# Kernel tuning notes

Hardware: AMD Instinct MI355X
Metric: run time of the kernel (lower is better)

## Reference

```python
import jax, jax.numpy as jnp
import numpy as np

# module hyperparameters (from init_kwargs)
STRIDE, PAD, DIL = 1, 1, 1
GROUPS, DG = 1, 1
KH, KW = 3, 3
CIN, COUT = 256, 256


def _mdcn_forward(x, offset, mask, weight, bias):
    B, C, H, W = x.shape
    Cout = weight.shape[0]
    K = KH * KW
    Ho = (H + 2 * PAD - (DIL * (KH - 1) + 1)) // STRIDE + 1
    Wo = (W + 2 * PAD - (DIL * (KW - 1) + 1)) // STRIDE + 1
    Cg = C // DG

    # offset channel layout: ((g*K + k)*2 + {0: dy, 1: dx})
    off = offset.reshape(B, DG, KH, KW, 2, Ho, Wo)
    base_y = (jnp.arange(Ho) * STRIDE - PAD)[None, :] + DIL * jnp.arange(KH)[:, None]  # [KH,Ho]
    base_x = (jnp.arange(Wo) * STRIDE - PAD)[None, :] + DIL * jnp.arange(KW)[:, None]  # [KW,Wo]
    sy = base_y[None, None, :, None, :, None].astype(x.dtype) + off[:, :, :, :, 0]  # [B,DG,KH,KW,Ho,Wo]
    sx = base_x[None, None, None, :, None, :].astype(x.dtype) + off[:, :, :, :, 1]

    y0f = jnp.floor(sy); x0f = jnp.floor(sx)
    wy = sy - y0f; wx = sx - x0f
    y0 = y0f.astype(jnp.int32); x0 = x0f.astype(jnp.int32)

    xg = x.reshape(B, DG, Cg, H * W)

    def corner(yc, xc, w):
        valid = (yc >= 0) & (yc < H) & (xc >= 0) & (xc < W)
        idx = jnp.clip(yc, 0, H - 1) * W + jnp.clip(xc, 0, W - 1)  # [B,DG,KH,KW,Ho,Wo]
        v = jnp.take_along_axis(xg, idx.reshape(B, DG, 1, -1), axis=3)  # [B,DG,Cg,K*Ho*Wo]
        v = v.reshape(B, DG, Cg, KH, KW, Ho, Wo)
        return v * (w * valid.astype(x.dtype))[:, :, None]

    val = (corner(y0, x0, (1 - wy) * (1 - wx))
           + corner(y0, x0 + 1, (1 - wy) * wx)
           + corner(y0 + 1, x0, wy * (1 - wx))
           + corner(y0 + 1, x0 + 1, wy * wx))  # [B,DG,Cg,KH,KW,Ho,Wo]

    cols = val * mask.reshape(B, DG, 1, KH, KW, Ho, Wo)
    cols = cols.reshape(B, GROUPS, (C // GROUPS) * K, Ho * Wo)
    wg = weight.reshape(GROUPS, Cout // GROUPS, (C // GROUPS) * K)
    out = jnp.einsum('gok,bgkp->bgop', wg, cols).reshape(B, Cout, Ho, Wo)
    return out + bias[None, :, None, None]


def setup_inputs() -> dict:
    key = jax.random.key(0)
    k1, k2, k3, k4 = jax.random.split(key, 4)
    B, H, W = 4, 64, 64
    x = jax.random.normal(k1, (B, CIN, H, W), dtype=jnp.float32)
    offset = jax.random.normal(k2, (B, 2 * DG * KH * KW, H, W), dtype=jnp.float32)
    mask = jax.random.uniform(k3, (B, DG * KH * KW, H, W), dtype=jnp.float32)
    stdv = 1.0 / np.sqrt(CIN * KH * KW)
    weight = jax.random.uniform(k4, (COUT, CIN // GROUPS, KH, KW), dtype=jnp.float32,
                                minval=-stdv, maxval=stdv)
    bias = jnp.zeros((COUT,), dtype=jnp.float32)
    return {"x": x, "offset": offset, "mask": mask, "weight": weight, "bias": bias}


def reference(x, offset, mask, weight, bias):
    return _mdcn_forward(x, offset, mask, weight, bias)
```

## Files before the change

kernel.cpp:

```cpp
#include <hip/hip_runtime.h>
#include <hip/hip_bf16.h>
#include <stdint.h>

#define KDIM 2304

typedef __bf16 bf16_t;
typedef bf16_t bf16x8 __attribute__((ext_vector_type(8)));
typedef float f32x4 __attribute__((ext_vector_type(4)));
typedef float f32x2 __attribute__((ext_vector_type(2)));

__device__ __forceinline__ float b2f_lo(uint32_t u) {
  union { uint32_t i; float f; } c; c.i = u << 16; return c.f;
}
__device__ __forceinline__ float b2f_hi(uint32_t u) {
  union { uint32_t i; float f; } c; c.i = u & 0xffff0000u; return c.f;
}
__device__ __forceinline__ uint32_t pk_bf16(float a, float b) {
  __hip_bfloat162 h = __float22bfloat162_rn(make_float2(a, b));
  union { __hip_bfloat162 h; uint32_t u; } c; c.h = h; return c.u;
}

__global__ __launch_bounds__(256) void k_prep(const float* __restrict__ x,
                                              uint16_t* __restrict__ xt,
                                              const float* __restrict__ w,
                                              uint16_t* __restrict__ wt2) {
  int tid = threadIdx.x;
  if (blockIdx.x < 2048) {
    __shared__ float tile[32][65];
    int b = blockIdx.x >> 9;
    int cgrp = (blockIdx.x >> 6) & 7;
    int sgrp = blockIdx.x & 63;
    int c0 = cgrp << 5, s0 = sgrp << 6;
#pragma unroll
    for (int it = 0; it < 2; ++it) {
      int f = tid + it * 256;
      int rr = f >> 4, col = (f & 15) << 2;
      float4 v = *(const float4*)&x[((size_t)(b * 256 + c0 + rr)) * 4096 + s0 + col];
      tile[rr][col + 0] = v.x;
      tile[rr][col + 1] = v.y;
      tile[rr][col + 2] = v.z;
      tile[rr][col + 3] = v.w;
    }
    __syncthreads();
    int sp = tid >> 2, cg = tid & 3;
    uint4 o;
    o.x = pk_bf16(tile[cg * 8 + 0][sp], tile[cg * 8 + 1][sp]);
    o.y = pk_bf16(tile[cg * 8 + 2][sp], tile[cg * 8 + 3][sp]);
    o.z = pk_bf16(tile[cg * 8 + 4][sp], tile[cg * 8 + 5][sp]);
    o.w = pk_bf16(tile[cg * 8 + 6][sp], tile[cg * 8 + 7][sp]);
    *(uint4*)&xt[((size_t)b * 4096 + s0 + sp) * 256 + c0 + cg * 8] = o;
  } else {
    __shared__ float wl[2304];
    int row = blockIdx.x - 2048;
    const float* wrow = w + (size_t)row * KDIM;
    for (int i2 = tid; i2 < 2304; i2 += 256) wl[i2] = wrow[i2];
    __syncthreads();
    int strip = row >> 4, r16 = row & 15;
    for (int c = tid; c < 288; c += 256) {
      int tap = c >> 5, rem = c & 31;
      int w64 = rem >> 3, kh = (rem >> 2) & 1, seg = rem & 3;
      int i = tap * 4 + w64;
      int cin0 = w64 * 64 + kh * 32 + seg * 8;
      int lanex = seg * 16 + r16;
      uint16_t* dst = wt2 + (size_t)i * 16384 + (size_t)(strip * 128 + kh * 64 + lanex) * 8;
      uint4 o;
      o.x = pk_bf16(wl[(cin0 + 0) * 9 + tap], wl[(cin0 + 1) * 9 + tap]);
      o.y = pk_bf16(wl[(cin0 + 2) * 9 + tap], wl[(cin0 + 3) * 9 + tap]);
      o.z = pk_bf16(wl[(cin0 + 4) * 9 + tap], wl[(cin0 + 5) * 9 + tap]);
      o.w = pk_bf16(wl[(cin0 + 6) * 9 + tap], wl[(cin0 + 7) * 9 + tap]);
      *(uint4*)dst = o;
    }
  }
}

__device__ __forceinline__ void mk_corners(int tap, int p, int ho,
                                           const float* s_off, const float* s_msk,
                                           float cw[4], int cpo[4]) {
  int kh = tap / 3, kw = tap - kh * 3;
  float dy = s_off[(2 * tap) * 64 + p];
  float dx = s_off[(2 * tap + 1) * 64 + p];
  float mm = s_msk[tap * 64 + p];
  float sy = (float)(ho - 1 + kh) + dy;
  float sx = (float)(p - 1 + kw) + dx;
  float fy = floorf(sy), fx = floorf(sx);
  int y0 = (int)fy, x0 = (int)fx;
  float wy = sy - fy, wx = sx - fx;
#pragma unroll
  for (int cy = 0; cy < 2; ++cy) {
#pragma unroll
    for (int cx = 0; cx < 2; ++cx) {
      int y = y0 + cy, xx = x0 + cx;
      float wgt = (cy ? wy : 1.f - wy) * (cx ? wx : 1.f - wx) * mm;
      bool v = ((unsigned)y < 64u) && ((unsigned)xx < 64u);
      wgt = v ? wgt : 0.f;
      int yc = min(max(y, 0), 63), xc = min(max(xx, 0), 63);
      cw[cy * 2 + cx] = wgt;
      cpo[cy * 2 + cx] = ((yc << 6) + xc) * 256;
    }
  }
}

__global__ __launch_bounds__(1024, 4) void k_fused(const uint16_t* __restrict__ xt,
                                                   const uint16_t* __restrict__ wt2,
                                                   const float* __restrict__ off,
                                                   const float* __restrict__ msk,
                                                   const float* __restrict__ bias,
                                                   float* __restrict__ out) {
  __shared__ __align__(16) uint16_t Bs[2][64][64];
  __shared__ float s_off[18 * 64];
  __shared__ float s_msk[9 * 64];

  int tid = threadIdx.x;
  int swz = ((int)blockIdx.x & 7) * 32 + ((int)blockIdx.x >> 3);
  int b = swz >> 6, ho = swz & 63;

  const float* offb = off + (size_t)b * 18 * 4096 + ho * 64;
  for (int i = tid; i < 18 * 64; i += 1024)
    s_off[i] = offb[(size_t)(i >> 6) * 4096 + (i & 63)];
  const float* mskb = msk + (size_t)b * 9 * 4096 + ho * 64;
  for (int i = tid; i < 9 * 64; i += 1024)
    s_msk[i] = mskb[(size_t)(i >> 6) * 4096 + (i & 63)];

  int lane = tid & 63, wv = tid >> 6;
  int wm = wv >> 1, wn = wv & 1;
  int q = lane >> 4, r = lane & 15;
  int p = tid >> 4, cg = tid & 15;
  const uint16_t* xtb = xt + (size_t)b * 4096 * 256 + cg * 4;
  int bcol = (((cg >> 1) ^ (p & 7)) << 3) + ((cg & 1) << 2);

  f32x4 acc[2][2];
#pragma unroll
  for (int mi = 0; mi < 2; ++mi)
#pragma unroll
    for (int ni = 0; ni < 2; ++ni) acc[mi][ni] = f32x4{0.f, 0.f, 0.f, 0.f};

  __syncthreads();

  float cw[4];
  int cpo[4];
  uint2 dnv[4];
  bf16x8 AFA[2][2], AFB[2][2];

  int c0 = (q ^ (r & 7)) << 3;
  int c1 = c0 ^ 32;
  int rb0 = (wn * 32 + r) * 64;

  mk_corners(0, p, ho, s_off, s_msk, cw, cpo);
#pragma unroll
  for (int c = 0; c < 4; ++c) dnv[c] = *(const uint2*)(xtb + cpo[c]);
  {
    const uint16_t* wp = wt2 + wm * 2048 + lane * 8;
    AFA[0][0] = *(const bf16x8*)(wp);
    AFA[0][1] = *(const bf16x8*)(wp + 512);
    AFA[1][0] = *(const bf16x8*)(wp + 1024);
    AFA[1][1] = *(const bf16x8*)(wp + 1536);
  }
  {
    f32x2 a0 = {0.f, 0.f}, a1 = {0.f, 0.f};
#pragma unroll
    for (int c = 0; c < 4; ++c) {
      f32x2 wc = {cw[c], cw[c]};
      a0 += wc * f32x2{b2f_lo(dnv[c].x), b2f_hi(dnv[c].x)};
      a1 += wc * f32x2{b2f_lo(dnv[c].y), b2f_hi(dnv[c].y)};
    }
    uint2 o;
    o.x = pk_bf16(a0.x, a0.y);
    o.y = pk_bf16(a1.x, a1.y);
    *(uint2*)&Bs[0][p][bcol] = o;
  }
  __syncthreads();

#define BODY(I, AFC, AFN, DOMK, DODNV, DOAF, DOBL)                              \
  {                                                                             \
    if (DOMK) mk_corners(((I) + 1) >> 2, p, ho, s_off, s_msk, cw, cpo);         \
    if (DODNV) {                                                                \
      const int chw = (((I) + 1) & 3) << 6;                                     \
      dnv[0] = *(const uint2*)(xtb + cpo[0] + chw);                             \
      dnv[1] = *(const uint2*)(xtb + cpo[1] + chw);                             \
      dnv[2] = *(const uint2*)(xtb + cpo[2] + chw);                             \
      dnv[3] = *(const uint2*)(xtb + cpo[3] + chw);                             \
    }                                                                           \
    if (DOAF) {                                                                 \
      const uint16_t* wp = wt2 + (size_t)((I) + 1) * 16384 + wm * 2048 + lane * 8; \
      AFN[0][0] = *(const bf16x8*)(wp);                                         \
      AFN[0][1] = *(const bf16x8*)(wp + 512);                                   \
      AFN[1][0] = *(const bf16x8*)(wp + 1024);                                  \
      AFN[1][1] = *(const bf16x8*)(wp + 1536);                                  \
    }                                                                           \
    {                                                                           \
      const uint16_t* bsrow = &Bs[(I) & 1][0][0];                               \
      bf16x8 b00 = *(const bf16x8*)(bsrow + rb0 + c0);           \
      bf16x8 b01 = *(const bf16x8*)(bsrow + rb0 + c1);           \
      bf16x8 b10 = *(const bf16x8*)(bsrow + rb0 + 1024 + c0);    \
      bf16x8 b11 = *(const bf16x8*)(bsrow + rb0 + 1024 + c1);    \
      __builtin_amdgcn_s_setprio(1);                                            \
      acc[0][0] = __builtin_amdgcn_mfma_f32_16x16x32_bf16(AFC[0][0], b00, acc[0][0], 0, 0, 0); \
      acc[0][1] = __builtin_amdgcn_mfma_f32_16x16x32_bf16(AFC[0][0], b10, acc[0][1], 0, 0, 0); \
      acc[1][0] = __builtin_amdgcn_mfma_f32_16x16x32_bf16(AFC[1][0], b00, acc[1][0], 0, 0, 0); \
      acc[1][1] = __builtin_amdgcn_mfma_f32_16x16x32_bf16(AFC[1][0], b10, acc[1][1], 0, 0, 0); \
      acc[0][0] = __builtin_amdgcn_mfma_f32_16x16x32_bf16(AFC[0][1], b01, acc[0][0], 0, 0, 0); \
      acc[0][1] = __builtin_amdgcn_mfma_f32_16x16x32_bf16(AFC[0][1], b11, acc[0][1], 0, 0, 0); \
      acc[1][0] = __builtin_amdgcn_mfma_f32_16x16x32_bf16(AFC[1][1], b01, acc[1][0], 0, 0, 0); \
      acc[1][1] = __builtin_amdgcn_mfma_f32_16x16x32_bf16(AFC[1][1], b11, acc[1][1], 0, 0, 0); \
      __builtin_amdgcn_s_setprio(0);                                            \
    }                                                                           \
    if (DOBL) {                                                                 \
      f32x2 a0 = {0.f, 0.f}, a1 = {0.f, 0.f};                                   \
      _Pragma("unroll")                                                         \
      for (int c = 0; c < 4; ++c) {                                             \
        f32x2 wc = {cw[c], cw[c]};                                              \
        a0 += wc * f32x2{b2f_lo(dnv[c].x), b2f_hi(dnv[c].x)};                   \
        a1 += wc * f32x2{b2f_lo(dnv[c].y), b2f_hi(dnv[c].y)};                   \
      }                                                                         \
      uint2 o;                                                                  \
      o.x = pk_bf16(a0.x, a0.y);                                                \
      o.y = pk_bf16(a1.x, a1.y);                                                \
      *(uint2*)&Bs[((I) + 1) & 1][p][bcol] = o;                                 \
    }                                                                           \
    __syncthreads();                                                            \
  }

#pragma unroll 1
  for (int ii = 0; ii < 8; ++ii) {
    int i0 = 4 * ii;
    BODY(i0 + 0, AFA, AFB, 0, 1, 1, 1)
    BODY(i0 + 1, AFB, AFA, 0, 1, 1, 1)
    BODY(i0 + 2, AFA, AFB, 0, 1, 1, 1)
    BODY(i0 + 3, AFB, AFA, 1, 1, 1, 1)
  }
  BODY(32, AFA, AFB, 0, 1, 1, 1)
  BODY(33, AFB, AFA, 0, 1, 1, 1)
  BODY(34, AFA, AFB, 0, 1, 1, 1)
  BODY(35, AFB, AFA, 0, 0, 0, 0)
#undef BODY

#pragma unroll
  for (int mi = 0; mi < 2; ++mi) {
#pragma unroll
    for (int j = 0; j < 4; ++j) {
      int m = wm * 32 + mi * 16 + q * 4 + j;
      float bv = bias[m];
#pragma unroll
      for (int ni = 0; ni < 2; ++ni) {
        int wog = wn * 32 + ni * 16 + r;
        out[((size_t)(b * 256 + m)) * 4096 + ho * 64 + wog] = acc[mi][ni][j] + bv;
      }
    }
  }
}

extern "C" void kernel_launch(void* const* d_in, const int* in_sizes, int n_in,
                              void* d_out, int out_size, void* d_ws, size_t ws_size,
                              hipStream_t stream) {
  (void)in_sizes; (void)n_in; (void)out_size; (void)ws_size;
  const float* x      = (const float*)d_in[0];
  const float* offset = (const float*)d_in[1];
  const float* mask   = (const float*)d_in[2];
  const float* weight = (const float*)d_in[3];
  const float* bias   = (const float*)d_in[4];
  float* out = (float*)d_out;

  uint8_t* ws = (uint8_t*)d_ws;
  uint16_t* xt  = (uint16_t*)ws;
  uint16_t* wt2 = (uint16_t*)(ws + 8388608);

  k_prep<<<dim3(2304), 256, 0, stream>>>(x, xt, weight, wt2);
  k_fused<<<dim3(256), 1024, 0, stream>>>(xt, wt2, offset, mask, bias, out);
}
```

Baseline: 130.7 us.

## Split output channels across two blocks per row with 512 threads

Each output row is now handled by two 512-thread blocks, each computing half of the 256 output channels, so the grid doubles to 512 blocks. Each thread gathers 8 channels with 16-byte loads instead of 4 channels with 8-byte loads, which halves the per-thread gather instruction count. The cost is that the bilinear sampling and column building is done twice per row, once in each block, which doubles gather traffic and interpolation work. In exchange, more blocks are available to fill the GPU's compute units.

```diff
diff --git a/kernel.cpp b/kernel.cpp
--- a/kernel.cpp
+++ b/kernel.cpp
@@ -100,33 +100,34 @@
   }
 }
 
-__global__ __launch_bounds__(1024, 4) void k_fused(const uint16_t* __restrict__ xt,
-                                                   const uint16_t* __restrict__ wt2,
-                                                   const float* __restrict__ off,
-                                                   const float* __restrict__ msk,
-                                                   const float* __restrict__ bias,
-                                                   float* __restrict__ out) {
+__global__ __launch_bounds__(512, 4) void k_fused(const uint16_t* __restrict__ xt,
+                                                  const uint16_t* __restrict__ wt2,
+                                                  const float* __restrict__ off,
+                                                  const float* __restrict__ msk,
+                                                  const float* __restrict__ bias,
+                                                  float* __restrict__ out) {
   __shared__ __align__(16) uint16_t Bs[2][64][64];
   __shared__ float s_off[18 * 64];
   __shared__ float s_msk[9 * 64];
 
   int tid = threadIdx.x;
-  int swz = ((int)blockIdx.x & 7) * 32 + ((int)blockIdx.x >> 3);
-  int b = swz >> 6, ho = swz & 63;
+  int swz = ((int)blockIdx.x & 7) * 64 + ((int)blockIdx.x >> 3);
+  int b = swz >> 7, ho = (swz >> 1) & 63, mh = swz & 1;
 
   const float* offb = off + (size_t)b * 18 * 4096 + ho * 64;
-  for (int i = tid; i < 18 * 64; i += 1024)
+  for (int i = tid; i < 18 * 64; i += 512)
     s_off[i] = offb[(size_t)(i >> 6) * 4096 + (i & 63)];
   const float* mskb = msk + (size_t)b * 9 * 4096 + ho * 64;
-  for (int i = tid; i < 9 * 64; i += 1024)
+  for (int i = tid; i < 9 * 64; i += 512)
     s_msk[i] = mskb[(size_t)(i >> 6) * 4096 + (i & 63)];
 
   int lane = tid & 63, wv = tid >> 6;
   int wm = wv >> 1, wn = wv & 1;
   int q = lane >> 4, r = lane & 15;
-  int p = tid >> 4, cg = tid & 15;
-  const uint16_t* xtb = xt + (size_t)b * 4096 * 256 + cg * 4;
-  int bcol = (((cg >> 1) ^ (p & 7)) << 3) + ((cg & 1) << 2);
+  int p = tid >> 3, cgh = tid & 7;
+  const uint16_t* xtb = xt + (size_t)b * 1048576 + cgh * 8;
+  int bcol = (cgh ^ (p & 7)) << 3;
+  int awb = (mh * 4 + wm) * 2048;
 
   f32x4 acc[2][2];
 #pragma unroll
@@ -138,7 +139,7 @@
 
   float cw[4];
   int cpo[4];
-  uint2 dnv[4];
+  uint4 dnv[4];
   bf16x8 AFA[2][2], AFB[2][2];
 
   int c0 = (q ^ (r & 7)) << 3;
@@ -147,26 +148,30 @@
 
   mk_corners(0, p, ho, s_off, s_msk, cw, cpo);
 #pragma unroll
-  for (int c = 0; c < 4; ++c) dnv[c] = *(const uint2*)(xtb + cpo[c]);
+  for (int c = 0; c < 4; ++c) dnv[c] = *(const uint4*)(xtb + cpo[c]);
   {
-    const uint16_t* wp = wt2 + wm * 2048 + lane * 8;
+    const uint16_t* wp = wt2 + awb + lane * 8;
     AFA[0][0] = *(const bf16x8*)(wp);
     AFA[0][1] = *(const bf16x8*)(wp + 512);
     AFA[1][0] = *(const bf16x8*)(wp + 1024);
     AFA[1][1] = *(const bf16x8*)(wp + 1536);
   }
   {
-    f32x2 a0 = {0.f, 0.f}, a1 = {0.f, 0.f};
+    f32x2 f0 = {0.f, 0.f}, f1 = {0.f, 0.f}, f2 = {0.f, 0.f}, f3 = {0.f, 0.f};
 #pragma unroll
     for (int c = 0; c < 4; ++c) {
       f32x2 wc = {cw[c], cw[c]};
-      a0 += wc * f32x2{b2f_lo(dnv[c].x), b2f_hi(dnv[c].x)};
-      a1 += wc * f32x2{b2f_lo(dnv[c].y), b2f_hi(dnv[c].y)};
-    }
-    uint2 o;
-    o.x = pk_bf16(a0.x, a0.y);
-    o.y = pk_bf16(a1.x, a1.y);
-    *(uint2*)&Bs[0][p][bcol] = o;
+      f0 += wc * f32x2{b2f_lo(dnv[c].x), b2f_hi(dnv[c].x)};
+      f1 += wc * f32x2{b2f_lo(dnv[c].y), b2f_hi(dnv[c].y)};
+      f2 += wc * f32x2{b2f_lo(dnv[c].z), b2f_hi(dnv[c].z)};
+      f3 += wc * f32x2{b2f_lo(dnv[c].w), b2f_hi(dnv[c].w)};
+    }
+    uint4 o;
+    o.x = pk_bf16(f0.x, f0.y);
+    o.y = pk_bf16(f1.x, f1.y);
+    o.z = pk_bf16(f2.x, f2.y);
+    o.w = pk_bf16(f3.x, f3.y);
+    *(uint4*)&Bs[0][p][bcol] = o;
   }
   __syncthreads();
 
@@ -175,13 +180,13 @@
     if (DOMK) mk_corners(((I) + 1) >> 2, p, ho, s_off, s_msk, cw, cpo);         \
     if (DODNV) {                                                                \
       const int chw = (((I) + 1) & 3) << 6;                                     \
-      dnv[0] = *(const uint2*)(xtb + cpo[0] + chw);                             \
-      dnv[1] = *(const uint2*)(xtb + cpo[1] + chw);                             \
-      dnv[2] = *(const uint2*)(xtb + cpo[2] + chw);                             \
-      dnv[3] = *(const uint2*)(xtb + cpo[3] + chw);                             \
+      dnv[0] = *(const uint4*)(xtb + cpo[0] + chw);                             \
+      dnv[1] = *(const uint4*)(xtb + cpo[1] + chw);                             \
+      dnv[2] = *(const uint4*)(xtb + cpo[2] + chw);                             \
+      dnv[3] = *(const uint4*)(xtb + cpo[3] + chw);                             \
     }                                                                           \
     if (DOAF) {                                                                 \
-      const uint16_t* wp = wt2 + (size_t)((I) + 1) * 16384 + wm * 2048 + lane * 8; \
+      const uint16_t* wp = wt2 + (size_t)((I) + 1) * 16384 + awb + lane * 8;    \
       AFN[0][0] = *(const bf16x8*)(wp);                                         \
       AFN[0][1] = *(const bf16x8*)(wp + 512);                                   \
       AFN[1][0] = *(const bf16x8*)(wp + 1024);                                  \
@@ -205,17 +210,21 @@
       __builtin_amdgcn_s_setprio(0);                                            \
     }                                                                           \
     if (DOBL) {                                                                 \
-      f32x2 a0 = {0.f, 0.f}, a1 = {0.f, 0.f};                                   \
+      f32x2 f0 = {0.f, 0.f}, f1 = {0.f, 0.f}, f2 = {0.f, 0.f}, f3 = {0.f, 0.f};\
       _Pragma("unroll")                                                         \
       for (int c = 0; c < 4; ++c) {                                             \
         f32x2 wc = {cw[c], cw[c]};                                              \
-        a0 += wc * f32x2{b2f_lo(dnv[c].x), b2f_hi(dnv[c].x)};                   \
-        a1 += wc * f32x2{b2f_lo(dnv[c].y), b2f_hi(dnv[c].y)};                   \
+        f0 += wc * f32x2{b2f_lo(dnv[c].x), b2f_hi(dnv[c].x)};                   \
+        f1 += wc * f32x2{b2f_lo(dnv[c].y), b2f_hi(dnv[c].y)};                   \
+        f2 += wc * f32x2{b2f_lo(dnv[c].z), b2f_hi(dnv[c].z)};                   \
+        f3 += wc * f32x2{b2f_lo(dnv[c].w), b2f_hi(dnv[c].w)};                   \
       }                                                                         \
-      uint2 o;                                                                  \
-      o.x = pk_bf16(a0.x, a0.y);                                                \
-      o.y = pk_bf16(a1.x, a1.y);                                                \
-      *(uint2*)&Bs[((I) + 1) & 1][p][bcol] = o;                                 \
+      uint4 o;                                                                  \
+      o.x = pk_bf16(f0.x, f0.y);                                                \
+      o.y = pk_bf16(f1.x, f1.y);                                                \
+      o.z = pk_bf16(f2.x, f2.y);                                                \
+      o.w = pk_bf16(f3.x, f3.y);                                                \
+      *(uint4*)&Bs[((I) + 1) & 1][p][bcol] = o;                                 \
     }                                                                           \
     __syncthreads();                                                            \
   }
@@ -238,7 +247,7 @@
   for (int mi = 0; mi < 2; ++mi) {
 #pragma unroll
     for (int j = 0; j < 4; ++j) {
-      int m = wm * 32 + mi * 16 + q * 4 + j;
+      int m = mh * 128 + wm * 32 + mi * 16 + q * 4 + j;
       float bv = bias[m];
 #pragma unroll
       for (int ni = 0; ni < 2; ++ni) {
@@ -265,5 +274,5 @@
   uint16_t* wt2 = (uint16_t*)(ws + 8388608);
 
   k_prep<<<dim3(2304), 256, 0, stream>>>(x, xt, weight, wt2);
-  k_fused<<<dim3(256), 1024, 0, stream>>>(xt, wt2, offset, mask, bias, out);
-}
+  k_fused<<<dim3(512), 512, 0, stream>>>(xt, wt2, offset, mask, bias, out);
+}
```

Result: no change. 128.5 us (-1.7%).
